# Optimization experiments

Measured on AMD Instinct MI355X. Metric: run time of the kernel, lower is better.

## Reference

```python
import jax, jax.numpy as jnp
import numpy as np

SEQ, IN, H = 64, 100000, 50


def setup_inputs() -> dict:
    key = jax.random.key(0)
    k0, k1, k2, k3, k4 = jax.random.split(key, 5)
    x = jax.random.normal(k0, (SEQ, 1, IN), dtype=jnp.float32) * 0.02
    Wi = jax.random.normal(k1, (IN, 4 * H), dtype=jnp.float32) * 0.01
    bi = jax.random.normal(k2, (4 * H,), dtype=jnp.float32) * 0.01
    Wh = jax.random.normal(k3, (H, 4 * H), dtype=jnp.float32) * 0.1
    bh = jax.random.normal(k4, (4 * H,), dtype=jnp.float32) * 0.01
    return {"x": x, "Wi": Wi, "bi": bi, "Wh": Wh, "bh": bh}


def reference(x, Wi, bi, Wh, bh):
    # x: [seq, batch=1, input_size] -- each row is a flattened ParameterList.
    # Precompute the input projection for all steps at once (one big GEMM),
    # same math as per-step input_weights(input) since it has no recurrence.
    gates_in = jnp.einsum('sbi,ig->sbg', x, Wi) + bi + bh  # [seq, 1, 4H]

    def step(carry, g_in):
        hx, cx = carry
        gates = g_in + hx @ Wh  # [1, 4H]
        i, f, g, o = jnp.split(gates, 4, axis=1)
        i = jax.nn.sigmoid(i)
        f = jax.nn.sigmoid(f)
        g = jnp.tanh(g)
        o = jax.nn.sigmoid(o)
        cy = f * cx + i * g
        hy = o * jnp.tanh(cy)
        return (hy, cy), None

    h0 = jnp.zeros((1, H), dtype=x.dtype)
    c0 = jnp.zeros((1, H), dtype=x.dtype)
    (h_final, _), _ = jax.lax.scan(step, (h0, c0), gates_in)
    # torch.squeeze(out_hidden): (1, H) -> (H,)
    return jnp.squeeze(h_final)
```

## Files before the change

### kernel.cpp

```cpp
#include <hip/hip_runtime.h>
#include <hip/hip_bf16.h>


#define K_DIM 100000
#define NG 200
#define NS 64
#define TK 32
#define NBLK 256
#define NTILES 3125
#define CELLS (NS * NG)
#define CELLS4 (CELLS / 4)
#define ROWU 40

typedef unsigned short u16;
typedef unsigned int   u32;
typedef __bf16 bf16x8 __attribute__((ext_vector_type(8)));
typedef float  f32x16 __attribute__((ext_vector_type(16)));

#define TILE_BARRIER() do {                                   \
    asm volatile("s_waitcnt lgkmcnt(0)" ::: "memory");        \
    __builtin_amdgcn_s_barrier();                             \
    __builtin_amdgcn_sched_barrier(0);                        \
} while (0)

static __device__ __forceinline__ u32 rne16(float f) {
    u32 u = __float_as_uint(f);
    return (u + 0x7FFFu + ((u >> 16) & 1u)) >> 16;
}
static __device__ __forceinline__ void split_hl(float f, u32& h, u32& l) {
    u32 u  = __float_as_uint(f);
    u32 hb = u & 0xFFFF0000u;
    h = hb >> 16;
    l = rne16(f - __uint_as_float(hb));
}
static __device__ __forceinline__ void split4(float4 v, u32 h[4], u32 l[4]) {
    split_hl(v.x, h[0], l[0]); split_hl(v.y, h[1], l[1]);
    split_hl(v.z, h[2], l[2]); split_hl(v.w, h[3], l[3]);
}
static __device__ __forceinline__ f32x16 mfma_bf(uint4 a, uint4 b, f32x16 c) {
    return __builtin_amdgcn_mfma_f32_32x32x16_bf16(
        __builtin_bit_cast(bf16x8, a), __builtin_bit_cast(bf16x8, b), c, 0, 0, 0);
}
static __device__ __forceinline__ float rl(float v, int j) {
    return __int_as_float(__builtin_amdgcn_readlane(__float_as_int(v), j));
}

__global__ __launch_bounds__(512, 1) void k1_gemm_partial(
    const float* __restrict__ x, const float* __restrict__ Wi,
    float* __restrict__ partial)
{
    __shared__ __align__(16) u16 WH[2][224 * ROWU];
    __shared__ __align__(16) u16 WL[2][224 * ROWU];
    __shared__ __align__(16) u16 XH[2][64 * ROWU];
    __shared__ __align__(16) u16 XL[2][64 * ROWU];

    const int t    = threadIdx.x;
    const int lane = t & 63;
    const int wave = t >> 6;
    const int m    = lane & 31;
    const int h    = lane >> 5;
    const int stile = wave >> 2;
    const int gset  = wave & 3;

#pragma unroll
    for (int b = 0; b < 2; ++b) {
        u32* zh = (u32*)&WH[b][200 * ROWU];
        u32* zl = (u32*)&WL[b][200 * ROWU];
        for (int i = t; i < 24 * ROWU / 2; i += 512) { zh[i] = 0; zl[i] = 0; }
    }

    const int a_g4 = t >> 3;
    const int a_k4 = t & 7;
    const bool has_w = (t < 400);
    const int xs0 = t >> 3, xk0 = t & 7;

    auto do_loads = [&](int ti, float4 (&wr)[4], float4& xr) {
        const size_t kt = (size_t)ti * TK;
        if (has_w) {
#pragma unroll
            for (int j = 0; j < 4; ++j)
                wr[j] = *(const float4*)(Wi + (kt + a_k4 * 4 + j) * NG + a_g4 * 4);
        }
        xr = *(const float4*)(x + (size_t)xs0 * K_DIM + kt + xk0 * 4);
    };
    auto stage_wi = [&](const float4 (&r)[4], u16* WHp, u16* WLp) {
        u32 hw[4][4], lw[4][4];
#pragma unroll
        for (int j = 0; j < 4; ++j) split4(r[j], hw[j], lw[j]);
#pragma unroll
        for (int j2 = 0; j2 < 4; ++j2) {
            int off = (4 * a_g4 + j2) * ROWU + a_k4 * 4;
            *(uint2*)&WHp[off] = make_uint2(hw[0][j2] | (hw[1][j2] << 16),
                                            hw[2][j2] | (hw[3][j2] << 16));
            *(uint2*)&WLp[off] = make_uint2(lw[0][j2] | (lw[1][j2] << 16),
                                            lw[2][j2] | (lw[3][j2] << 16));
        }
    };
    auto stage_x = [&](float4 v, u16* XHp, u16* XLp) {
        u32 hh[4], ll[4];
        split4(v, hh, ll);
        int off = xs0 * ROWU + xk0 * 4;
        *(uint2*)&XHp[off] = make_uint2(hh[0] | (hh[1] << 16), hh[2] | (hh[3] << 16));
        *(uint2*)&XLp[off] = make_uint2(ll[0] | (ll[1] << 16), ll[2] | (ll[3] << 16));
    };

    f32x16 acc[2];
#pragma unroll
    for (int tt = 0; tt < 2; ++tt)
#pragma unroll
        for (int r = 0; r < 16; ++r) acc[tt][r] = 0.f;

    const int aoff = (stile * 32 + m) * ROWU + h * 8;
    int boff[2];
#pragma unroll
    for (int tt = 0; tt < 2; ++tt) {
        int gt = (gset == 3 && tt == 1) ? 6 : (2 * gset + tt);
        boff[tt] = (gt * 32 + m) * ROWU + h * 8;
    }

    auto mfma_phase = [&](int p) {
        const u16* WHp = WH[p]; const u16* WLp = WL[p];
        const u16* XHp = XH[p]; const u16* XLp = XL[p];
#pragma unroll
        for (int kk = 0; kk < 2; ++kk) {
            uint4 ah = *(const uint4*)&XHp[aoff + kk * 16];
            uint4 al = *(const uint4*)&XLp[aoff + kk * 16];
#pragma unroll
            for (int tt = 0; tt < 2; ++tt) {
                uint4 bh = *(const uint4*)&WHp[boff[tt] + kk * 16];
                uint4 bl = *(const uint4*)&WLp[boff[tt] + kk * 16];
                acc[tt] = mfma_bf(ah, bh, acc[tt]);
                acc[tt] = mfma_bf(ah, bl, acc[tt]);
                acc[tt] = mfma_bf(al, bh, acc[tt]);
            }
        }
    };

    float4 waA[4], waB[4];
    float4 xaA, xaB;
    const int ti0 = blockIdx.x;
    do_loads(ti0,            waA, xaA);
    do_loads(ti0 + NBLK,     waB, xaB);
    if (has_w) stage_wi(waA, WH[0], WL[0]);
    stage_x(xaA, XH[0], XL[0]);
    do_loads(ti0 + 2 * NBLK, waA, xaA);
    TILE_BARRIER();

    int p = 0;
    int ti = ti0;
    while (ti < NTILES) {
        {
            int tn = ti + NBLK;
            if (tn < NTILES) {
                if (has_w) stage_wi(waB, WH[p ^ 1], WL[p ^ 1]);
                stage_x(xaB, XH[p ^ 1], XL[p ^ 1]);
                int tf = tn + 2 * NBLK;
                if (tf < NTILES) do_loads(tf, waB, xaB);
            }
            mfma_phase(p);
            TILE_BARRIER();
            p ^= 1; ti += NBLK;
        }
        if (ti >= NTILES) break;
        {
            int tn = ti + NBLK;
            if (tn < NTILES) {
                if (has_w) stage_wi(waA, WH[p ^ 1], WL[p ^ 1]);
                stage_x(xaA, XH[p ^ 1], XL[p ^ 1]);
                int tf = tn + 2 * NBLK;
                if (tf < NTILES) do_loads(tf, waA, xaA);
            }
            mfma_phase(p);
            TILE_BARRIER();
            p ^= 1; ti += NBLK;
        }
    }

    float* base = partial + (size_t)blockIdx.x * CELLS;
#pragma unroll
    for (int tt = 0; tt < 2; ++tt) {
        if (gset == 3 && tt == 1) continue;
        int g = (2 * gset + tt) * 32 + m;
        if (g < NG) {
#pragma unroll
            for (int r = 0; r < 16; ++r) {
                int srow = stile * 32 + (r & 3) + 8 * (r >> 2) + 4 * h;
                base[srow * NG + g] = acc[tt][r];
            }
        }
    }
}

__global__ __launch_bounds__(512) void k2_reduce(
    const float* __restrict__ partial, const float* __restrict__ bi,
    const float* __restrict__ bh, float* __restrict__ gates)
{
    __shared__ float4 red[512];
    const int tid   = threadIdx.x;
    const int fid   = tid & 15;
    const int slice = tid >> 4;
    const int g4    = blockIdx.x * 16 + fid;

    const float4* p4 = (const float4*)partial;
    float4 sum = make_float4(0.f, 0.f, 0.f, 0.f);
#pragma unroll 4
    for (int b = slice * 8; b < slice * 8 + 8; ++b) {
        float4 v = p4[(size_t)b * CELLS4 + g4];
        sum.x += v.x; sum.y += v.y; sum.z += v.z; sum.w += v.w;
    }
    red[tid] = sum;
    __syncthreads();
    if (tid < 16) {
        float4 tot = red[tid];
#pragma unroll
        for (int p = 1; p < 32; ++p) {
            float4 v = red[p * 16 + tid];
            tot.x += v.x; tot.y += v.y; tot.z += v.z; tot.w += v.w;
        }
        int gg = (g4 * 4) % NG;
        float4 b1 = *(const float4*)(bi + gg);
        float4 b2 = *(const float4*)(bh + gg);
        tot.x += b1.x + b2.x; tot.y += b1.y + b2.y;
        tot.z += b1.z + b2.z; tot.w += b1.w + b2.w;
        ((float4*)gates)[g4] = tot;
    }
}

__global__ __launch_bounds__(256)
__attribute__((amdgpu_waves_per_eu(1)))
void k3_lstm(
    const float* __restrict__ gates, const float* __restrict__ Wh,
    float* __restrict__ out)
{
    __shared__ float act[2][NG];
    const int tid = threadIdx.x;
    const int w   = tid >> 6;
    const int l   = tid & 63;
    const bool al = (l < 50);
    const int  lc = al ? l : 49;
    const int  gidx = w * 50 + lc;

    float wv[50];
#pragma unroll
    for (int j = 0; j < 50; ++j) wv[j] = Wh[j * NG + gidx];

    const float* gp = gates + gidx;
    float gz = gp[0];
    float c = 0.f, h = 0.f;

    for (int s = 0; s < 64; ++s) {
        float nz = (s < 63) ? gp[(s + 1) * NG] : 0.f;

        float a0 = gz, a1 = 0.f, a2 = 0.f, a3 = 0.f;
#pragma unroll
        for (int j = 0; j < 48; j += 4) {
            a0 = fmaf(rl(h, j),     wv[j],     a0);
            a1 = fmaf(rl(h, j + 1), wv[j + 1], a1);
            a2 = fmaf(rl(h, j + 2), wv[j + 2], a2);
            a3 = fmaf(rl(h, j + 3), wv[j + 3], a3);
        }
        a0 = fmaf(rl(h, 48), wv[48], a0);
        a1 = fmaf(rl(h, 49), wv[49], a1);
        float z = (a0 + a1) + (a2 + a3);

        float e = __expf(-z);
        float av;
        if (w == 2) { float e2 = e * e; av = (1.f - e2) / (1.f + e2); }
        else        { av = 1.f / (1.f + e); }
        if (al) act[s & 1][gidx] = av;

        TILE_BARRIER();

        float iv = act[s & 1][lc];
        float fv = act[s & 1][50 + lc];
        float gv = act[s & 1][100 + lc];
        float ov = act[s & 1][150 + lc];
        c = fmaf(fv, c, iv * gv);
        float e2c = __expf(-2.f * c);
        h = ov * (1.f - e2c) / (1.f + e2c);

        gz = nz;
    }
    if (w == 0 && al) out[l] = h;
}

extern "C" void kernel_launch(void* const* d_in, const int* in_sizes, int n_in,
                              void* d_out, int out_size, void* d_ws, size_t ws_size,
                              hipStream_t stream)
{
    const float* x  = (const float*)d_in[0];
    const float* Wi = (const float*)d_in[1];
    const float* bi = (const float*)d_in[2];
    const float* Wh = (const float*)d_in[3];
    const float* bh = (const float*)d_in[4];
    float* out = (float*)d_out;

    float* partial = (float*)d_ws;
    float* gates   = partial + (size_t)NBLK * CELLS;

    k1_gemm_partial<<<NBLK, 512, 0, stream>>>(x, Wi, partial);
    k2_reduce<<<CELLS4 / 16, 512, 0, stream>>>(partial, bi, bh, gates);
    k3_lstm<<<1, 256, 0, stream>>>(gates, Wh, out);
}
```

Measured before the change: 177.6 us.

## Use 512 smaller single-buffered GEMM blocks with two occupancy per CU

```diff
diff --git a/kernel.cpp b/kernel.cpp
--- a/kernel.cpp
+++ b/kernel.cpp
@@ -6,7 +6,7 @@
 #define NG 200
 #define NS 64
 #define TK 32
-#define NBLK 256
+#define NBLK 512
 #define NTILES 3125
 #define CELLS (NS * NG)
 #define CELLS4 (CELLS / 4)
@@ -45,72 +45,79 @@
     return __int_as_float(__builtin_amdgcn_readlane(__float_as_int(v), j));
 }
 
-__global__ __launch_bounds__(512, 1) void k1_gemm_partial(
+__global__ __launch_bounds__(256, 2) void k1_gemm_partial(
     const float* __restrict__ x, const float* __restrict__ Wi,
     float* __restrict__ partial)
 {
-    __shared__ __align__(16) u16 WH[2][224 * ROWU];
-    __shared__ __align__(16) u16 WL[2][224 * ROWU];
-    __shared__ __align__(16) u16 XH[2][64 * ROWU];
-    __shared__ __align__(16) u16 XL[2][64 * ROWU];
+    __shared__ __align__(16) u16 WH[224 * ROWU];
+    __shared__ __align__(16) u16 WL[224 * ROWU];
+    __shared__ __align__(16) u16 XH[64 * ROWU];
+    __shared__ __align__(16) u16 XL[64 * ROWU];
 
     const int t    = threadIdx.x;
     const int lane = t & 63;
-    const int wave = t >> 6;
+    const int gset = t >> 6;
     const int m    = lane & 31;
     const int h    = lane >> 5;
-    const int stile = wave >> 2;
-    const int gset  = wave & 3;
-
-#pragma unroll
-    for (int b = 0; b < 2; ++b) {
-        u32* zh = (u32*)&WH[b][200 * ROWU];
-        u32* zl = (u32*)&WL[b][200 * ROWU];
-        for (int i = t; i < 24 * ROWU / 2; i += 512) { zh[i] = 0; zl[i] = 0; }
-    }
-
-    const int a_g4 = t >> 3;
-    const int a_k4 = t & 7;
-    const bool has_w = (t < 400);
-    const int xs0 = t >> 3, xk0 = t & 7;
-
-    auto do_loads = [&](int ti, float4 (&wr)[4], float4& xr) {
+
+    {
+        u32* zh = (u32*)&WH[200 * ROWU];
+        u32* zl = (u32*)&WL[200 * ROWU];
+        for (int i = t; i < 24 * ROWU / 2; i += 256) { zh[i] = 0; zl[i] = 0; }
+    }
+
+    const int g4a = t >> 3,         k4a = t & 7;
+    const int g4b = (t + 256) >> 3, k4b = t & 7;
+    const bool hw2 = (t < 144);
+    const int xk  = t & 7;
+    const int xsA = t >> 3;
+    const int xsB = xsA + 32;
+
+    auto do_loads = [&](int ti, float4 (&w0)[4], float4 (&w1)[4],
+                        float4& x0, float4& x1) {
         const size_t kt = (size_t)ti * TK;
-        if (has_w) {
+#pragma unroll
+        for (int j = 0; j < 4; ++j)
+            w0[j] = *(const float4*)(Wi + (kt + k4a * 4 + j) * NG + g4a * 4);
+        if (hw2) {
 #pragma unroll
             for (int j = 0; j < 4; ++j)
-                wr[j] = *(const float4*)(Wi + (kt + a_k4 * 4 + j) * NG + a_g4 * 4);
-        }
-        xr = *(const float4*)(x + (size_t)xs0 * K_DIM + kt + xk0 * 4);
+                w1[j] = *(const float4*)(Wi + (kt + k4b * 4 + j) * NG + g4b * 4);
+        }
+        x0 = *(const float4*)(x + (size_t)xsA * K_DIM + kt + xk * 4);
+        x1 = *(const float4*)(x + (size_t)xsB * K_DIM + kt + xk * 4);
     };
-    auto stage_wi = [&](const float4 (&r)[4], u16* WHp, u16* WLp) {
+    auto stage_wi = [&](const float4 (&r)[4], int g4, int k4) {
         u32 hw[4][4], lw[4][4];
 #pragma unroll
         for (int j = 0; j < 4; ++j) split4(r[j], hw[j], lw[j]);
 #pragma unroll
         for (int j2 = 0; j2 < 4; ++j2) {
-            int off = (4 * a_g4 + j2) * ROWU + a_k4 * 4;
-            *(uint2*)&WHp[off] = make_uint2(hw[0][j2] | (hw[1][j2] << 16),
-                                            hw[2][j2] | (hw[3][j2] << 16));
-            *(uint2*)&WLp[off] = make_uint2(lw[0][j2] | (lw[1][j2] << 16),
-                                            lw[2][j2] | (lw[3][j2] << 16));
+            int off = (4 * g4 + j2) * ROWU + k4 * 4;
+            *(uint2*)&WH[off] = make_uint2(hw[0][j2] | (hw[1][j2] << 16),
+                                           hw[2][j2] | (hw[3][j2] << 16));
+            *(uint2*)&WL[off] = make_uint2(lw[0][j2] | (lw[1][j2] << 16),
+                                           lw[2][j2] | (lw[3][j2] << 16));
         }
     };
-    auto stage_x = [&](float4 v, u16* XHp, u16* XLp) {
+    auto stage_x = [&](float4 v, int s) {
         u32 hh[4], ll[4];
         split4(v, hh, ll);
-        int off = xs0 * ROWU + xk0 * 4;
-        *(uint2*)&XHp[off] = make_uint2(hh[0] | (hh[1] << 16), hh[2] | (hh[3] << 16));
-        *(uint2*)&XLp[off] = make_uint2(ll[0] | (ll[1] << 16), ll[2] | (ll[3] << 16));
+        int off = s * ROWU + xk * 4;
+        *(uint2*)&XH[off] = make_uint2(hh[0] | (hh[1] << 16), hh[2] | (hh[3] << 16));
+        *(uint2*)&XL[off] = make_uint2(ll[0] | (ll[1] << 16), ll[2] | (ll[3] << 16));
     };
 
-    f32x16 acc[2];
-#pragma unroll
-    for (int tt = 0; tt < 2; ++tt)
-#pragma unroll
-        for (int r = 0; r < 16; ++r) acc[tt][r] = 0.f;
-
-    const int aoff = (stile * 32 + m) * ROWU + h * 8;
+    f32x16 acc[2][2];
+#pragma unroll
+    for (int st = 0; st < 2; ++st)
+#pragma unroll
+        for (int tt = 0; tt < 2; ++tt)
+#pragma unroll
+            for (int r = 0; r < 16; ++r) acc[st][tt][r] = 0.f;
+
+    const int aoff0 = (0 * 32 + m) * ROWU + h * 8;
+    const int aoff1 = (1 * 32 + m) * ROWU + h * 8;
     int boff[2];
 #pragma unroll
     for (int tt = 0; tt < 2; ++tt) {
@@ -118,74 +125,73 @@
         boff[tt] = (gt * 32 + m) * ROWU + h * 8;
     }
 
-    auto mfma_phase = [&](int p) {
-        const u16* WHp = WH[p]; const u16* WLp = WL[p];
-        const u16* XHp = XH[p]; const u16* XLp = XL[p];
+    auto mfma_phase = [&]() {
 #pragma unroll
         for (int kk = 0; kk < 2; ++kk) {
-            uint4 ah = *(const uint4*)&XHp[aoff + kk * 16];
-            uint4 al = *(const uint4*)&XLp[aoff + kk * 16];
+            uint4 a0h = *(const uint4*)&XH[aoff0 + kk * 16];
+            uint4 a0l = *(const uint4*)&XL[aoff0 + kk * 16];
+            uint4 a1h = *(const uint4*)&XH[aoff1 + kk * 16];
+            uint4 a1l = *(const uint4*)&XL[aoff1 + kk * 16];
 #pragma unroll
             for (int tt = 0; tt < 2; ++tt) {
-                uint4 bh = *(const uint4*)&WHp[boff[tt] + kk * 16];
-                uint4 bl = *(const uint4*)&WLp[boff[tt] + kk * 16];
-                acc[tt] = mfma_bf(ah, bh, acc[tt]);
-                acc[tt] = mfma_bf(ah, bl, acc[tt]);
-                acc[tt] = mfma_bf(al, bh, acc[tt]);
+                uint4 bh = *(const uint4*)&WH[boff[tt] + kk * 16];
+                uint4 bl = *(const uint4*)&WL[boff[tt] + kk * 16];
+                acc[0][tt] = mfma_bf(a0h, bh, acc[0][tt]);
+                acc[0][tt] = mfma_bf(a0h, bl, acc[0][tt]);
+                acc[0][tt] = mfma_bf(a0l, bh, acc[0][tt]);
+                acc[1][tt] = mfma_bf(a1h, bh, acc[1][tt]);
+                acc[1][tt] = mfma_bf(a1h, bl, acc[1][tt]);
+                acc[1][tt] = mfma_bf(a1l, bh, acc[1][tt]);
             }
         }
     };
 
-    float4 waA[4], waB[4];
-    float4 xaA, xaB;
+    float4 wA0[4], wA1[4], wB0[4], wB1[4];
+    float4 xA0, xA1, xB0, xB1;
     const int ti0 = blockIdx.x;
-    do_loads(ti0,            waA, xaA);
-    do_loads(ti0 + NBLK,     waB, xaB);
-    if (has_w) stage_wi(waA, WH[0], WL[0]);
-    stage_x(xaA, XH[0], XL[0]);
-    do_loads(ti0 + 2 * NBLK, waA, xaA);
-    TILE_BARRIER();
-
-    int p = 0;
+    do_loads(ti0,        wA0, wA1, xA0, xA1);
+    do_loads(ti0 + NBLK, wB0, wB1, xB0, xB1);
+
     int ti = ti0;
     while (ti < NTILES) {
         {
-            int tn = ti + NBLK;
-            if (tn < NTILES) {
-                if (has_w) stage_wi(waB, WH[p ^ 1], WL[p ^ 1]);
-                stage_x(xaB, XH[p ^ 1], XL[p ^ 1]);
-                int tf = tn + 2 * NBLK;
-                if (tf < NTILES) do_loads(tf, waB, xaB);
-            }
-            mfma_phase(p);
+            stage_wi(wA0, g4a, k4a);
+            if (hw2) stage_wi(wA1, g4b, k4b);
+            stage_x(xA0, xsA); stage_x(xA1, xsB);
+            int tf = ti + 2 * NBLK;
+            if (tf < NTILES) do_loads(tf, wA0, wA1, xA0, xA1);
             TILE_BARRIER();
-            p ^= 1; ti += NBLK;
+            mfma_phase();
+            TILE_BARRIER();
+            ti += NBLK;
         }
         if (ti >= NTILES) break;
         {
-            int tn = ti + NBLK;
-            if (tn < NTILES) {
-                if (has_w) stage_wi(waA, WH[p ^ 1], WL[p ^ 1]);
-                stage_x(xaA, XH[p ^ 1], XL[p ^ 1]);
-                int tf = tn + 2 * NBLK;
-                if (tf < NTILES) do_loads(tf, waA, xaA);
-            }
-            mfma_phase(p);
+            stage_wi(wB0, g4a, k4a);
+            if (hw2) stage_wi(wB1, g4b, k4b);
+            stage_x(xB0, xsA); stage_x(xB1, xsB);
+            int tf = ti + 2 * NBLK;
+            if (tf < NTILES) do_loads(tf, wB0, wB1, xB0, xB1);
             TILE_BARRIER();
-            p ^= 1; ti += NBLK;
+            mfma_phase();
+            TILE_BARRIER();
+            ti += NBLK;
         }
     }
 
     float* base = partial + (size_t)blockIdx.x * CELLS;
 #pragma unroll
-    for (int tt = 0; tt < 2; ++tt) {
-        if (gset == 3 && tt == 1) continue;
-        int g = (2 * gset + tt) * 32 + m;
-        if (g < NG) {
-#pragma unroll
-            for (int r = 0; r < 16; ++r) {
-                int srow = stile * 32 + (r & 3) + 8 * (r >> 2) + 4 * h;
-                base[srow * NG + g] = acc[tt][r];
+    for (int st = 0; st < 2; ++st) {
+#pragma unroll
+        for (int tt = 0; tt < 2; ++tt) {
+            if (gset == 3 && tt == 1) continue;
+            int g = (2 * gset + tt) * 32 + m;
+            if (g < NG) {
+#pragma unroll
+                for (int r = 0; r < 16; ++r) {
+                    int srow = st * 32 + (r & 3) + 8 * (r >> 2) + 4 * h;
+                    base[srow * NG + g] = acc[st][tt][r];
+                }
             }
         }
     }
@@ -204,7 +210,7 @@
     const float4* p4 = (const float4*)partial;
     float4 sum = make_float4(0.f, 0.f, 0.f, 0.f);
 #pragma unroll 4
-    for (int b = slice * 8; b < slice * 8 + 8; ++b) {
+    for (int b = slice * 16; b < slice * 16 + 16; ++b) {
         float4 v = p4[(size_t)b * CELLS4 + g4];
         sum.x += v.x; sum.y += v.y; sum.z += v.z; sum.w += v.w;
     }
@@ -298,7 +304,7 @@
     float* partial = (float*)d_ws;
     float* gates   = partial + (size_t)NBLK * CELLS;
 
-    k1_gemm_partial<<<NBLK, 512, 0, stream>>>(x, Wi, partial);
+    k1_gemm_partial<<<NBLK, 256, 0, stream>>>(x, Wi, partial);
     k2_reduce<<<CELLS4 / 16, 512, 0, stream>>>(partial, bi, bh, gates);
     k3_lstm<<<1, 256, 0, stream>>>(gates, Wh, out);
 }
```

Measured after the change: 184.0 us. +3.6%, slower.
